# Kernel tuning notes

Hardware: AMD Instinct MI355X
Metric: run time of the kernel (lower is better)

The kernel has to match this reference:

```python
import jax, jax.numpy as jnp
import numpy as np

B, S, DM, H = 4, 4096, 1024, 16
HD = DM // H

def setup_inputs() -> dict:
    key = jax.random.key(0)
    ks = jax.random.split(key, 9)
    sc = 1.0 / np.sqrt(DM)
    return {
        "x": jax.random.normal(ks[0], (B, S, DM), dtype=jnp.float32),
        "Wq": jax.random.normal(ks[1], (DM, DM), dtype=jnp.float32) * sc,
        "bq": jnp.zeros((DM,), dtype=jnp.float32),
        "Wk": jax.random.normal(ks[2], (DM, DM), dtype=jnp.float32) * sc,
        "bk": jnp.zeros((DM,), dtype=jnp.float32),
        "Wv": jax.random.normal(ks[3], (DM, DM), dtype=jnp.float32) * sc,
        "bv": jnp.zeros((DM,), dtype=jnp.float32),
        "Wo": jax.random.normal(ks[4], (DM, DM), dtype=jnp.float32) * sc,
        "bo": jnp.zeros((DM,), dtype=jnp.float32),
    }

def _heads(t):
    # [B,S,DM] -> [B,H,S,HD]
    return t.reshape(B, S, H, HD).transpose(0, 2, 1, 3)

def reference(x, Wq, bq, Wk, bk, Wv, bv, Wo, bo):
    q = _heads(x @ Wq.T + bq)
    k = _heads(x @ Wk.T + bk)
    v = _heads(x @ Wv.T + bv)
    q = jax.nn.elu(q) + 1.0  # positive feature map
    k = jax.nn.elu(k) + 1.0
    # kv aggregation: [B,H,HD,HD]
    kv = jnp.einsum('bhsd,bhse->bhde', k, v)
    qkv = jnp.einsum('bhsd,bhde->bhse', q, kv)  # [B,H,S,HD]
    k_sum = k.sum(axis=2)  # [B,H,HD]
    normalizer = jnp.einsum('bhsd,bhd->bhs', q, k_sum) + 1e-6
    out = qkv / normalizer[..., None]
    out = out.transpose(0, 2, 1, 3).reshape(B, S, DM)
    return out @ Wo.T + bo  # dropout is identity in eval
```

## Files before the change

### kernel.cpp

```cpp
#include <hip/hip_runtime.h>
#include <math.h>

#define NROWS  16384
#define DMODEL 1024
#define NHEAD  16
#define HDIM   64
#define SEQ    4096
#define NBATCH 4
#define NBH    64
#define SCHUNK 16
#define M1     1048576u

typedef __attribute__((ext_vector_type(8))) short bf16x8;
typedef __attribute__((ext_vector_type(4))) float f32x4;

__device__ __forceinline__ unsigned short f2bf(float f) {
    unsigned u = __float_as_uint(f);
    u += 0x7FFFu + ((u >> 16) & 1u);
    return (unsigned short)(u >> 16);
}
__device__ __forceinline__ float bf2f(unsigned short h) {
    return __uint_as_float((unsigned)h << 16);
}

__device__ __forceinline__ void gload16(const void* g, void* l) {
    __builtin_amdgcn_global_load_lds(
        (const __attribute__((address_space(1))) unsigned int*)g,
        (__attribute__((address_space(3))) unsigned int*)l, 16, 0, 0);
}

__global__ __launch_bounds__(256)
void split_pair(const float* __restrict__ a, unsigned short* __restrict__ hi,
                unsigned short* __restrict__ lo, int n4)
{
    int i = blockIdx.x * 256 + threadIdx.x;
    const int stride = gridDim.x * 256;
    for (; i < n4; i += stride) {
        const float4 v = ((const float4*)a)[i];
        ushort4 H, L;
        H.x = f2bf(v.x); L.x = f2bf(v.x - bf2f(H.x));
        H.y = f2bf(v.y); L.y = f2bf(v.y - bf2f(H.y));
        H.z = f2bf(v.z); L.z = f2bf(v.z - bf2f(H.z));
        H.w = f2bf(v.w); L.w = f2bf(v.w - bf2f(H.w));
        ((ushort4*)hi)[i] = H;
        ((ushort4*)lo)[i] = L;
    }
}

__global__ __launch_bounds__(256)
void split_w4(const float* __restrict__ a0, const float* __restrict__ a1,
              const float* __restrict__ a2, const float* __restrict__ a3,
              unsigned short* __restrict__ dst)
{
    const int y = blockIdx.y;
    const float* src = (y == 0) ? a0 : (y == 1) ? a1 : (y == 2) ? a2 : a3;
    unsigned short* hi = dst + (size_t)y * 2u * M1;
    unsigned short* lo = hi + M1;
    const int i = blockIdx.x * 256 + threadIdx.x;
    const float4 v = ((const float4*)src)[i];
    ushort4 H, L;
    H.x = f2bf(v.x); L.x = f2bf(v.x - bf2f(H.x));
    H.y = f2bf(v.y); L.y = f2bf(v.y - bf2f(H.y));
    H.z = f2bf(v.z); L.z = f2bf(v.z - bf2f(H.z));
    H.w = f2bf(v.w); L.w = f2bf(v.w - bf2f(H.w));
    ((ushort4*)hi)[i] = H;
    ((ushort4*)lo)[i] = L;
}

template<int ELU>
__global__ __launch_bounds__(512)
void gemm_split8(const unsigned short* __restrict__ Ah, const unsigned short* __restrict__ Al,
                 const unsigned short* __restrict__ Wh, const unsigned short* __restrict__ Wl,
                 const float* __restrict__ bias, float* __restrict__ C)
{
    __shared__ unsigned short lds[2 * 32768];
    const int t    = threadIdx.x;
    const int lane = t & 63;
    const int wv   = t >> 6;
    const int wr   = wv >> 2;
    const int wcn  = wv & 3;

    const int bid  = blockIdx.x;
    const int swz  = ((bid & 7) << 5) | (bid >> 3);
    const int am0  = (swz >> 2) * 256;
    const int bn0  = (swz & 3) * 256;

    const int srow = lane >> 2;
    const int scol = (lane & 3) * 8;
    const int fr   = lane & 15;
    const int j0   = lane >> 4;

    f32x4 acc[8][4];
#pragma unroll
    for (int i = 0; i < 8; ++i)
#pragma unroll
        for (int j = 0; j < 4; ++j)
#pragma unroll
            for (int e = 0; e < 4; ++e) acc[i][j][e] = 0.f;

    auto stage = [&](int ph, int k0, unsigned wb) {
        const unsigned short* gs = (ph == 0) ? Ah : (ph == 1) ? Al : (ph == 2) ? Wh : Wl;
        const int rbase = (ph < 2) ? am0 : bn0;
#pragma unroll
        for (int c = 0; c < 2; ++c) {
            const int grow = rbase + c * 128 + wv * 16 + srow;
            gload16(gs + (size_t)grow * DMODEL + k0 + scol,
                    (unsigned short*)&lds[wb + (unsigned)ph * 8192u + (unsigned)(c * 128 + wv * 16) * 32u]);
        }
    };

#pragma unroll
    for (int ph = 0; ph < 4; ++ph) stage(ph, 0, 0u);
    __syncthreads();

    for (int ks = 0; ks < 32; ++ks) {
        const unsigned rb = (ks & 1) ? 32768u : 0u;
        const unsigned wb = rb ^ 32768u;
        const int k0n = (ks + 1) * 32;
        const bool pf = (ks < 31);

        bf16x8 bh[4], bl[4];
#pragma unroll
        for (int ph = 0; ph < 4; ++ph) {
            if (ph == 0) {
#pragma unroll
                for (int j = 0; j < 4; ++j) {
                    const unsigned ro = (unsigned)(wcn * 64 + j * 16 + fr) * 32u + (unsigned)j0 * 8u;
                    bh[j] = *(const bf16x8*)&lds[rb + 16384u + ro];
                    bl[j] = *(const bf16x8*)&lds[rb + 24576u + ro];
                }
            }
            bf16x8 a_h[2], a_l[2];
#pragma unroll
            for (int i2 = 0; i2 < 2; ++i2) {
                const unsigned ro = (unsigned)(wr * 128 + (ph * 2 + i2) * 16 + fr) * 32u + (unsigned)j0 * 8u;
                a_h[i2] = *(const bf16x8*)&lds[rb + ro];
                a_l[i2] = *(const bf16x8*)&lds[rb + 8192u + ro];
            }
            if (pf) stage(ph, k0n, wb);
            __builtin_amdgcn_s_barrier();
            __builtin_amdgcn_s_setprio(1);
#pragma unroll
            for (int i2 = 0; i2 < 2; ++i2)
#pragma unroll
                for (int j = 0; j < 4; ++j) {
                    acc[ph * 2 + i2][j] = __builtin_amdgcn_mfma_f32_16x16x32_bf16(a_h[i2], bh[j], acc[ph * 2 + i2][j], 0, 0, 0);
                    acc[ph * 2 + i2][j] = __builtin_amdgcn_mfma_f32_16x16x32_bf16(a_h[i2], bl[j], acc[ph * 2 + i2][j], 0, 0, 0);
                    acc[ph * 2 + i2][j] = __builtin_amdgcn_mfma_f32_16x16x32_bf16(a_l[i2], bh[j], acc[ph * 2 + i2][j], 0, 0, 0);
                }
            __builtin_amdgcn_s_setprio(0);
            if (ph < 3) __builtin_amdgcn_s_barrier();
        }
        __syncthreads();
    }

    const int crow0 = am0 + wr * 128 + (lane >> 4) * 4;
    const int ccol0 = bn0 + wcn * 64 + fr;
#pragma unroll
    for (int j = 0; j < 4; ++j) {
        const int col = ccol0 + j * 16;
        const float bv = bias[col];
#pragma unroll
        for (int i = 0; i < 8; ++i) {
            const int row = crow0 + i * 16;
#pragma unroll
            for (int r = 0; r < 4; ++r) {
                float v = acc[i][j][r] + bv;
                if (ELU) v = (v > 0.f) ? (v + 1.f) : __expf(v);
                C[(size_t)(row + r) * DMODEL + col] = v;
            }
        }
    }
}

__global__ __launch_bounds__(512)
void kv_partial(const float* __restrict__ k, const float* __restrict__ v,
                float* __restrict__ kvp, float* __restrict__ ksp)
{
    __shared__ float Ks[32][64];
    __shared__ float Vs[32][64];
    const int t  = threadIdx.x;
    const int bh = blockIdx.x;
    const int b  = bh >> 4;
    const int h  = bh & 15;
    const int sc = blockIdx.y;
    const int d  = t & 63;
    const int e0 = (t >> 6) * 8;

    float acc[8];
#pragma unroll
    for (int j = 0; j < 8; ++j) acc[j] = 0.f;
    float ks = 0.f;

    const size_t rowbase = (size_t)b * SEQ;
    const int sbeg = sc * (SEQ / SCHUNK);
    const int send = sbeg + (SEQ / SCHUNK);
    const int lrow = t >> 4;
    const int lc4  = (t & 15) * 4;

    for (int s0 = sbeg; s0 < send; s0 += 32) {
        const size_t g = (rowbase + s0 + lrow) * DMODEL + h * HDIM + lc4;
        *(float4*)&Ks[lrow][lc4] = *(const float4*)&k[g];
        *(float4*)&Vs[lrow][lc4] = *(const float4*)&v[g];
        __syncthreads();
#pragma unroll 8
        for (int sp = 0; sp < 32; ++sp) {
            const float kd = Ks[sp][d];
            if (t < 64) ks += Ks[sp][t];
            const float4 v0 = *(const float4*)&Vs[sp][e0 + 0];
            const float4 v1 = *(const float4*)&Vs[sp][e0 + 4];
            acc[0] = fmaf(kd, v0.x, acc[0]);  acc[1] = fmaf(kd, v0.y, acc[1]);
            acc[2] = fmaf(kd, v0.z, acc[2]);  acc[3] = fmaf(kd, v0.w, acc[3]);
            acc[4] = fmaf(kd, v1.x, acc[4]);  acc[5] = fmaf(kd, v1.y, acc[5]);
            acc[6] = fmaf(kd, v1.z, acc[6]);  acc[7] = fmaf(kd, v1.w, acc[7]);
        }
        __syncthreads();
    }

    const size_t base = ((size_t)sc * NBH + bh) * HDIM;
    float4 o0; o0.x = acc[0]; o0.y = acc[1]; o0.z = acc[2]; o0.w = acc[3];
    float4 o1; o1.x = acc[4]; o1.y = acc[5]; o1.z = acc[6]; o1.w = acc[7];
    *(float4*)&kvp[(base + d) * HDIM + e0 + 0] = o0;
    *(float4*)&kvp[(base + d) * HDIM + e0 + 4] = o1;
    if (t < 64) ksp[base + t] = ks;
}

__global__ __launch_bounds__(256)
void kv_reduce(const float* __restrict__ kvp, const float* __restrict__ ksp,
               float* __restrict__ kv, float* __restrict__ ksum)
{
    const int i = blockIdx.x * 256 + threadIdx.x;
    const int NKV = NBH * HDIM * HDIM;
    if (i < NKV) {
        float s = 0.f;
#pragma unroll
        for (int c = 0; c < SCHUNK; ++c) s += kvp[(size_t)c * NKV + i];
        kv[i] = s;
    }
    if (i < NBH * HDIM) {
        float s = 0.f;
#pragma unroll
        for (int c = 0; c < SCHUNK; ++c) s += ksp[(size_t)c * NBH * HDIM + i];
        ksum[i] = s;
    }
}

__global__ __launch_bounds__(256)
void qkv_norm(const float* __restrict__ q, const float* __restrict__ kv,
              const float* __restrict__ ksum,
              unsigned short* __restrict__ ah, unsigned short* __restrict__ al)
{
    __shared__ float Qs[64][68];
    __shared__ float KVs[64][64];
    __shared__ float kss[64];
    const int t  = threadIdx.x;
    const int s0 = blockIdx.x * 64;
    const int b  = blockIdx.y;
    const int h  = blockIdx.z;
    const int bh = b * NHEAD + h;

#pragma unroll
    for (int i = 0; i < 4; ++i) {
        const int idx = i * 256 + t;
        const int row = idx >> 4;
        const int c4  = (idx & 15) * 4;
        const float4 vq = *(const float4*)&q[((size_t)b * SEQ + s0 + row) * DMODEL + h * HDIM + c4];
        *(float4*)&Qs[row][c4] = vq;
        *(float4*)&((float*)KVs)[idx * 4] = *(const float4*)&kv[(size_t)bh * HDIM * HDIM + idx * 4];
    }
    if (t < 64) kss[t] = ksum[(size_t)bh * HDIM + t];
    __syncthreads();

    const int r  = t >> 2;
    const int e0 = (t & 3) * 16;
    float out[16];
#pragma unroll
    for (int j = 0; j < 16; ++j) out[j] = 0.f;
    float nrm = 0.f;

#pragma unroll 8
    for (int d = 0; d < 64; ++d) {
        const float qd = Qs[r][d];
        nrm = fmaf(qd, kss[d], nrm);
        const float4 k0 = *(const float4*)&KVs[d][e0 + 0];
        const float4 k1 = *(const float4*)&KVs[d][e0 + 4];
        const float4 k2 = *(const float4*)&KVs[d][e0 + 8];
        const float4 k3 = *(const float4*)&KVs[d][e0 + 12];
        out[0]  = fmaf(qd, k0.x, out[0]);  out[1]  = fmaf(qd, k0.y, out[1]);
        out[2]  = fmaf(qd, k0.z, out[2]);  out[3]  = fmaf(qd, k0.w, out[3]);
        out[4]  = fmaf(qd, k1.x, out[4]);  out[5]  = fmaf(qd, k1.y, out[5]);
        out[6]  = fmaf(qd, k1.z, out[6]);  out[7]  = fmaf(qd, k1.w, out[7]);
        out[8]  = fmaf(qd, k2.x, out[8]);  out[9]  = fmaf(qd, k2.y, out[9]);
        out[10] = fmaf(qd, k2.z, out[10]); out[11] = fmaf(qd, k2.w, out[11]);
        out[12] = fmaf(qd, k3.x, out[12]); out[13] = fmaf(qd, k3.y, out[13]);
        out[14] = fmaf(qd, k3.z, out[14]); out[15] = fmaf(qd, k3.w, out[15]);
    }

    const float inv = 1.f / (nrm + 1e-6f);
    const size_t gbase = ((size_t)b * SEQ + s0 + r) * DMODEL + h * HDIM + e0;
#pragma unroll
    for (int g4 = 0; g4 < 4; ++g4) {
        ushort4 H, L;
        const float v0 = out[g4*4+0] * inv;
        const float v1 = out[g4*4+1] * inv;
        const float v2 = out[g4*4+2] * inv;
        const float v3 = out[g4*4+3] * inv;
        H.x = f2bf(v0); L.x = f2bf(v0 - bf2f(H.x));
        H.y = f2bf(v1); L.y = f2bf(v1 - bf2f(H.y));
        H.z = f2bf(v2); L.z = f2bf(v2 - bf2f(H.z));
        H.w = f2bf(v3); L.w = f2bf(v3 - bf2f(H.w));
        *(ushort4*)&ah[gbase + g4 * 4] = H;
        *(ushort4*)&al[gbase + g4 * 4] = L;
    }
}

extern "C" void kernel_launch(void* const* d_in, const int* in_sizes, int n_in,
                              void* d_out, int out_size, void* d_ws, size_t ws_size,
                              hipStream_t stream)
{
    const float* x  = (const float*)d_in[0];
    const float* Wq = (const float*)d_in[1];
    const float* bq = (const float*)d_in[2];
    const float* Wk = (const float*)d_in[3];
    const float* bk = (const float*)d_in[4];
    const float* Wv = (const float*)d_in[5];
    const float* bv = (const float*)d_in[6];
    const float* Wo = (const float*)d_in[7];
    const float* bo = (const float*)d_in[8];

    unsigned short* xh = (unsigned short*)d_ws;
    unsigned short* xl = xh + (size_t)NROWS * DMODEL;
    unsigned short* wsp = xl + (size_t)NROWS * DMODEL;
    float* buf0 = (float*)(wsp + 8u * M1);
    float* kv   = buf0 + (size_t)NROWS * DMODEL;
    float* ksum = kv + NBH * HDIM * HDIM;
    float* kvp  = ksum + NBH * HDIM;
    float* ksp  = kvp + (size_t)SCHUNK * NBH * HDIM * HDIM;
    float* vbuf = (float*)d_out;

    const dim3 gg(256);
    const int n4x = NROWS * DMODEL / 4;

    split_w4<<<dim3(1024, 4), 256, 0, stream>>>(Wq, Wk, Wv, Wo, wsp);
    split_pair<<<4096, 256, 0, stream>>>(x, xh, xl, n4x);
    gemm_split8<1><<<gg, 512, 0, stream>>>(xh, xl, wsp + 2u * M1, wsp + 3u * M1, bk, buf0);
    gemm_split8<0><<<gg, 512, 0, stream>>>(xh, xl, wsp + 4u * M1, wsp + 5u * M1, bv, vbuf);
    kv_partial<<<dim3(NBH, SCHUNK), 512, 0, stream>>>(buf0, vbuf, kvp, ksp);
    kv_reduce<<<1024, 256, 0, stream>>>(kvp, ksp, kv, ksum);
    gemm_split8<1><<<gg, 512, 0, stream>>>(xh, xl, wsp, wsp + M1, bq, buf0);
    qkv_norm<<<dim3(SEQ / 64, NBATCH, NHEAD), 256, 0, stream>>>(buf0, kv, ksum, xh, xl);
    gemm_split8<0><<<gg, 512, 0, stream>>>(xh, xl, wsp + 6u * M1, wsp + 7u * M1, bo, (float*)d_out);
}
```

Measured before the change: 485.5 us.

## Interleave hi/lo bf16 splits per row and run split GEMM as K=3072 loop

Stores the hi and lo bf16 parts of each row contiguously (row stride 2048) for x, the weights and the attention output. The GEMM then walks a concatenated K of 3072, pairing A=[hi,lo,hi] with W=[hi,hi,lo], with 64-wide K tiles and an XOR-swizzled LDS layout. This removes the per-step separate hi/lo loads and is meant to reduce LDS bank conflicts, though the MFMA count stays the same. It adds index arithmetic and changes the prefetch schedule across the four phases.

```diff
diff --git a/kernel.cpp b/kernel.cpp
--- a/kernel.cpp
+++ b/kernel.cpp
@@ -9,7 +9,7 @@
 #define NBATCH 4
 #define NBH    64
 #define SCHUNK 16
-#define M1     1048576u
+#define W1     2097152u
 
 typedef __attribute__((ext_vector_type(8))) short bf16x8;
 typedef __attribute__((ext_vector_type(4))) float f32x4;
@@ -30,50 +30,48 @@
 }
 
 __global__ __launch_bounds__(256)
-void split_pair(const float* __restrict__ a, unsigned short* __restrict__ hi,
-                unsigned short* __restrict__ lo, int n4)
-{
-    int i = blockIdx.x * 256 + threadIdx.x;
-    const int stride = gridDim.x * 256;
-    for (; i < n4; i += stride) {
-        const float4 v = ((const float4*)a)[i];
-        ushort4 H, L;
-        H.x = f2bf(v.x); L.x = f2bf(v.x - bf2f(H.x));
-        H.y = f2bf(v.y); L.y = f2bf(v.y - bf2f(H.y));
-        H.z = f2bf(v.z); L.z = f2bf(v.z - bf2f(H.z));
-        H.w = f2bf(v.w); L.w = f2bf(v.w - bf2f(H.w));
-        ((ushort4*)hi)[i] = H;
-        ((ushort4*)lo)[i] = L;
-    }
-}
-
-__global__ __launch_bounds__(256)
-void split_w4(const float* __restrict__ a0, const float* __restrict__ a1,
-              const float* __restrict__ a2, const float* __restrict__ a3,
-              unsigned short* __restrict__ dst)
-{
-    const int y = blockIdx.y;
-    const float* src = (y == 0) ? a0 : (y == 1) ? a1 : (y == 2) ? a2 : a3;
-    unsigned short* hi = dst + (size_t)y * 2u * M1;
-    unsigned short* lo = hi + M1;
-    const int i = blockIdx.x * 256 + threadIdx.x;
-    const float4 v = ((const float4*)src)[i];
+void split_x(const float* __restrict__ a, unsigned short* __restrict__ dst)
+{
+    const int idx = blockIdx.x * 256 + threadIdx.x;
+    const int row = idx >> 8;
+    const int c4  = (idx & 255) * 4;
+    const float4 v = ((const float4*)a)[idx];
     ushort4 H, L;
     H.x = f2bf(v.x); L.x = f2bf(v.x - bf2f(H.x));
     H.y = f2bf(v.y); L.y = f2bf(v.y - bf2f(H.y));
     H.z = f2bf(v.z); L.z = f2bf(v.z - bf2f(H.z));
     H.w = f2bf(v.w); L.w = f2bf(v.w - bf2f(H.w));
-    ((ushort4*)hi)[i] = H;
-    ((ushort4*)lo)[i] = L;
+    *(ushort4*)&dst[(size_t)row * 2048 + c4]        = H;
+    *(ushort4*)&dst[(size_t)row * 2048 + 1024 + c4] = L;
+}
+
+__global__ __launch_bounds__(256)
+void split_w4(const float* __restrict__ a0, const float* __restrict__ a1,
+              const float* __restrict__ a2, const float* __restrict__ a3,
+              unsigned short* __restrict__ dst)
+{
+    const int y = blockIdx.y;
+    const float* src = (y == 0) ? a0 : (y == 1) ? a1 : (y == 2) ? a2 : a3;
+    unsigned short* d = dst + (size_t)y * W1;
+    const int idx = blockIdx.x * 256 + threadIdx.x;
+    const int row = idx >> 8;
+    const int c4  = (idx & 255) * 4;
+    const float4 v = ((const float4*)src)[idx];
+    ushort4 H, L;
+    H.x = f2bf(v.x); L.x = f2bf(v.x - bf2f(H.x));
+    H.y = f2bf(v.y); L.y = f2bf(v.y - bf2f(H.y));
+    H.z = f2bf(v.z); L.z = f2bf(v.z - bf2f(H.z));
+    H.w = f2bf(v.w); L.w = f2bf(v.w - bf2f(H.w));
+    *(ushort4*)&d[(size_t)row * 2048 + c4]        = H;
+    *(ushort4*)&d[(size_t)row * 2048 + 1024 + c4] = L;
 }
 
 template<int ELU>
 __global__ __launch_bounds__(512)
-void gemm_split8(const unsigned short* __restrict__ Ah, const unsigned short* __restrict__ Al,
-                 const unsigned short* __restrict__ Wh, const unsigned short* __restrict__ Wl,
-                 const float* __restrict__ bias, float* __restrict__ C)
-{
-    __shared__ unsigned short lds[2 * 32768];
+void gemm_c3(const unsigned short* __restrict__ A2, const unsigned short* __restrict__ W2,
+             const float* __restrict__ bias, float* __restrict__ C)
+{
+    __shared__ unsigned short lds[65536];
     const int t    = threadIdx.x;
     const int lane = t & 63;
     const int wv   = t >> 6;
@@ -85,10 +83,11 @@
     const int am0  = (swz >> 2) * 256;
     const int bn0  = (swz & 3) * 256;
 
-    const int srow = lane >> 2;
-    const int scol = (lane & 3) * 8;
     const int fr   = lane & 15;
     const int j0   = lane >> 4;
+    const int fx   = lane & 7;
+    const int srow8 = lane >> 3;
+    const int sslot = (lane & 7) ^ srow8;
 
     f32x4 acc[8][4];
 #pragma unroll
@@ -98,58 +97,71 @@
 #pragma unroll
             for (int e = 0; e < 4; ++e) acc[i][j][e] = 0.f;
 
-    auto stage = [&](int ph, int k0, unsigned wb) {
-        const unsigned short* gs = (ph == 0) ? Ah : (ph == 1) ? Al : (ph == 2) ? Wh : Wl;
-        const int rbase = (ph < 2) ? am0 : bn0;
+    auto stageQ = [&](int q, int kt, unsigned wbU) {
+        const int k0 = kt * 64;
+        const bool isA = (q < 2);
+        const int kb  = isA ? ((k0 < 1024) ? k0 : k0 - 1024)
+                            : ((k0 < 2048) ? k0 : k0 - 2048);
+        const unsigned short* src = isA ? A2 : W2;
+        const int rb0 = (isA ? am0 : bn0) + (q & 1) * 128;
+        const unsigned ldsT = wbU + (isA ? 0u : 16384u) + (unsigned)((q & 1) * 128) * 64u;
 #pragma unroll
         for (int c = 0; c < 2; ++c) {
-            const int grow = rbase + c * 128 + wv * 16 + srow;
-            gload16(gs + (size_t)grow * DMODEL + k0 + scol,
-                    (unsigned short*)&lds[wb + (unsigned)ph * 8192u + (unsigned)(c * 128 + wv * 16) * 32u]);
+            const int r = rb0 + wv * 16 + c * 8 + srow8;
+            gload16(src + (size_t)r * 2048 + kb + sslot * 8,
+                    (unsigned short*)&lds[ldsT + (unsigned)(wv * 16 + c * 8) * 64u]);
         }
     };
 
 #pragma unroll
-    for (int ph = 0; ph < 4; ++ph) stage(ph, 0, 0u);
+    for (int q = 0; q < 4; ++q) stageQ(q, 0, 0u);
     __syncthreads();
 
-    for (int ks = 0; ks < 32; ++ks) {
-        const unsigned rb = (ks & 1) ? 32768u : 0u;
-        const unsigned wb = rb ^ 32768u;
-        const int k0n = (ks + 1) * 32;
-        const bool pf = (ks < 31);
-
-        bf16x8 bh[4], bl[4];
-#pragma unroll
-        for (int ph = 0; ph < 4; ++ph) {
-            if (ph == 0) {
-#pragma unroll
-                for (int j = 0; j < 4; ++j) {
-                    const unsigned ro = (unsigned)(wcn * 64 + j * 16 + fr) * 32u + (unsigned)j0 * 8u;
-                    bh[j] = *(const bf16x8*)&lds[rb + 16384u + ro];
-                    bl[j] = *(const bf16x8*)&lds[rb + 24576u + ro];
+    for (int kt = 0; kt < 48; ++kt) {
+        const unsigned rbU = (kt & 1) ? 32768u : 0u;
+        const unsigned wbU = rbU ^ 32768u;
+        const bool pf = (kt < 47);
+
+        bf16x8 bfr[2][4];
+#pragma unroll
+        for (int p = 0; p < 4; ++p) {
+            if (p == 0) {
+#pragma unroll
+                for (int h = 0; h < 2; ++h)
+#pragma unroll
+                    for (int j = 0; j < 4; ++j) {
+                        const unsigned phys = (unsigned)((h * 4 + j0) ^ fx);
+                        bfr[h][j] = *(const bf16x8*)&lds[rbU + 16384u +
+                            (unsigned)(wcn * 64 + j * 16 + fr) * 64u + phys * 8u];
+                    }
+            }
+            bf16x8 afr[2][2];
+#pragma unroll
+            for (int i2 = 0; i2 < 2; ++i2) {
+                const unsigned ar = (unsigned)(wr * 128 + (p * 2 + i2) * 16 + fr);
+#pragma unroll
+                for (int h = 0; h < 2; ++h) {
+                    const unsigned phys = (unsigned)((h * 4 + j0) ^ fx);
+                    afr[i2][h] = *(const bf16x8*)&lds[rbU + ar * 64u + phys * 8u];
                 }
             }
-            bf16x8 a_h[2], a_l[2];
-#pragma unroll
-            for (int i2 = 0; i2 < 2; ++i2) {
-                const unsigned ro = (unsigned)(wr * 128 + (ph * 2 + i2) * 16 + fr) * 32u + (unsigned)j0 * 8u;
-                a_h[i2] = *(const bf16x8*)&lds[rb + ro];
-                a_l[i2] = *(const bf16x8*)&lds[rb + 8192u + ro];
+            if (pf) {
+                if (p == 0) { stageQ(0, kt + 1, wbU); stageQ(1, kt + 1, wbU); }
+                else if (p == 1) stageQ(2, kt + 1, wbU);
+                else if (p == 2) stageQ(3, kt + 1, wbU);
             }
-            if (pf) stage(ph, k0n, wb);
             __builtin_amdgcn_s_barrier();
             __builtin_amdgcn_s_setprio(1);
 #pragma unroll
             for (int i2 = 0; i2 < 2; ++i2)
 #pragma unroll
-                for (int j = 0; j < 4; ++j) {
-                    acc[ph * 2 + i2][j] = __builtin_amdgcn_mfma_f32_16x16x32_bf16(a_h[i2], bh[j], acc[ph * 2 + i2][j], 0, 0, 0);
-                    acc[ph * 2 + i2][j] = __builtin_amdgcn_mfma_f32_16x16x32_bf16(a_h[i2], bl[j], acc[ph * 2 + i2][j], 0, 0, 0);
-                    acc[ph * 2 + i2][j] = __builtin_amdgcn_mfma_f32_16x16x32_bf16(a_l[i2], bh[j], acc[ph * 2 + i2][j], 0, 0, 0);
-                }
+                for (int j = 0; j < 4; ++j)
+#pragma unroll
+                    for (int h = 0; h < 2; ++h)
+                        acc[p * 2 + i2][j] = __builtin_amdgcn_mfma_f32_16x16x32_bf16(
+                            afr[i2][h], bfr[h][j], acc[p * 2 + i2][j], 0, 0, 0);
             __builtin_amdgcn_s_setprio(0);
-            if (ph < 3) __builtin_amdgcn_s_barrier();
+            if (p < 3) __builtin_amdgcn_s_barrier();
         }
         __syncthreads();
     }
@@ -247,8 +259,7 @@
 
 __global__ __launch_bounds__(256)
 void qkv_norm(const float* __restrict__ q, const float* __restrict__ kv,
-              const float* __restrict__ ksum,
-              unsigned short* __restrict__ ah, unsigned short* __restrict__ al)
+              const float* __restrict__ ksum, unsigned short* __restrict__ att)
 {
     __shared__ float Qs[64][68];
     __shared__ float KVs[64][64];
@@ -297,7 +308,7 @@
     }
 
     const float inv = 1.f / (nrm + 1e-6f);
-    const size_t gbase = ((size_t)b * SEQ + s0 + r) * DMODEL + h * HDIM + e0;
+    const size_t gb = ((size_t)b * SEQ + s0 + r) * 2048 + h * HDIM + e0;
 #pragma unroll
     for (int g4 = 0; g4 < 4; ++g4) {
         ushort4 H, L;
@@ -309,8 +320,8 @@
         H.y = f2bf(v1); L.y = f2bf(v1 - bf2f(H.y));
         H.z = f2bf(v2); L.z = f2bf(v2 - bf2f(H.z));
         H.w = f2bf(v3); L.w = f2bf(v3 - bf2f(H.w));
-        *(ushort4*)&ah[gbase + g4 * 4] = H;
-        *(ushort4*)&al[gbase + g4 * 4] = L;
+        *(ushort4*)&att[gb + g4 * 4]        = H;
+        *(ushort4*)&att[gb + 1024 + g4 * 4] = L;
     }
 }
 
@@ -328,10 +339,9 @@
     const float* Wo = (const float*)d_in[7];
     const float* bo = (const float*)d_in[8];
 
-    unsigned short* xh = (unsigned short*)d_ws;
-    unsigned short* xl = xh + (size_t)NROWS * DMODEL;
-    unsigned short* wsp = xl + (size_t)NROWS * DMODEL;
-    float* buf0 = (float*)(wsp + 8u * M1);
+    unsigned short* xs  = (unsigned short*)d_ws;
+    unsigned short* wsp = xs + (size_t)NROWS * 2048;
+    float* buf0 = (float*)(wsp + 4u * W1);
     float* kv   = buf0 + (size_t)NROWS * DMODEL;
     float* ksum = kv + NBH * HDIM * HDIM;
     float* kvp  = ksum + NBH * HDIM;
@@ -339,15 +349,14 @@
     float* vbuf = (float*)d_out;
 
     const dim3 gg(256);
-    const int n4x = NROWS * DMODEL / 4;
 
     split_w4<<<dim3(1024, 4), 256, 0, stream>>>(Wq, Wk, Wv, Wo, wsp);
-    split_pair<<<4096, 256, 0, stream>>>(x, xh, xl, n4x);
-    gemm_split8<1><<<gg, 512, 0, stream>>>(xh, xl, wsp + 2u * M1, wsp + 3u * M1, bk, buf0);
-    gemm_split8<0><<<gg, 512, 0, stream>>>(xh, xl, wsp + 4u * M1, wsp + 5u * M1, bv, vbuf);
+    split_x<<<16384, 256, 0, stream>>>(x, xs);
+    gemm_c3<1><<<gg, 512, 0, stream>>>(xs, wsp + 1u * W1, bk, buf0);
+    gemm_c3<0><<<gg, 512, 0, stream>>>(xs, wsp + 2u * W1, bv, vbuf);
     kv_partial<<<dim3(NBH, SCHUNK), 512, 0, stream>>>(buf0, vbuf, kvp, ksp);
     kv_reduce<<<1024, 256, 0, stream>>>(kvp, ksp, kv, ksum);
-    gemm_split8<1><<<gg, 512, 0, stream>>>(xh, xl, wsp, wsp + M1, bq, buf0);
-    qkv_norm<<<dim3(SEQ / 64, NBATCH, NHEAD), 256, 0, stream>>>(buf0, kv, ksum, xh, xl);
-    gemm_split8<0><<<gg, 512, 0, stream>>>(xh, xl, wsp + 6u * M1, wsp + 7u * M1, bo, (float*)d_out);
-}
+    gemm_c3<1><<<gg, 512, 0, stream>>>(xs, wsp, bq, buf0);
+    qkv_norm<<<dim3(SEQ / 64, NBATCH, NHEAD), 256, 0, stream>>>(buf0, kv, ksum, xs);
+    gemm_c3<0><<<gg, 512, 0, stream>>>(xs, wsp + 3u * W1, bo, (float*)d_out);
+}
```

Measured after the change: 522.8 us. +7.7%, slower.
